# Performance work log

Measured on AMD Instinct MI355X. Metric: run time of the kernel, lower is better.

The kernel has to match this reference:

```python
import jax, jax.numpy as jnp
import numpy as np

L, B, T, I, H, P, O = 2, 64, 512, 512, 512, 256, 512


def setup_inputs() -> dict:
    key = jax.random.key(0)
    ks = iter(jax.random.split(key, 40))
    SCALE = 0.03  # keep gate pre-activations in a sane range

    def w(shape):
        return jax.random.normal(next(ks), shape, jnp.float32) * SCALE

    return {
        "x": jax.random.normal(next(ks), (B, T, I), jnp.float32),
        "Wr": w((L, H, I + H)), "br": jnp.zeros((L, H), jnp.float32),
        "Wu": w((L, H, I + H)), "bu": jnp.ones((L, H), jnp.float32),  # update_gate bias init to 1.0
        "Wn": w((L, H, I + H)), "bn": jnp.zeros((L, H), jnp.float32),
        "Wmr": w((L, P, H)), "bmr": jnp.zeros((L, P), jnp.float32),
        "Wmw": w((L, P, H)), "bmw": jnp.zeros((L, P), jnp.float32),
        "Wmu": w((L, P, H)), "bmu": jnp.zeros((L, P), jnp.float32),
        "Wmh": w((L, H, P)), "bmh": jnp.zeros((L, H), jnp.float32),
        "Wd": w((L, P, H)), "bd": jnp.zeros((L, P), jnp.float32),
        "Ws": w((L, P, H)), "bs": jnp.zeros((L, P), jnp.float32),
        "Wout": w((O, H)), "bout": jnp.zeros((O,), jnp.float32),
        "dopamine": jnp.full((1,), 0.5, jnp.float32),
        "serotonin": jnp.full((1,), 0.5, jnp.float32),
    }


def _lin(x, W, b):
    # x: [B, in], W: [out, in] (torch Linear layout), b: [out]
    return jnp.einsum("bi,oi->bo", x, W) + b


def reference(x, Wr, br, Wu, bu, Wn, bn, Wmr, bmr, Wmw, bmw, Wmu, bmu,
              Wmh, bmh, Wd, bd, Ws, bs, Wout, bout, dopamine, serotonin):
    num_layers = Wr.shape[0]
    bsz = x.shape[0]
    hdim = Wr.shape[1]
    pdim = Wmr.shape[1]
    h0 = jnp.zeros((num_layers, bsz, hdim), x.dtype)
    m0 = jnp.zeros((num_layers, bsz, pdim), x.dtype)

    def step(carry, x_t):
        hidden, memory = carry  # [L,B,H], [L,B,P]
        inp = x_t
        new_h, new_m = [], []
        for l in range(num_layers):
            h, m = hidden[l], memory[l]
            comb = jnp.concatenate([inp, h], axis=-1)
            reset = jax.nn.sigmoid(_lin(comb, Wr[l], br[l]))
            update = jax.nn.sigmoid(_lin(comb, Wu[l], bu[l]))
            comb_r = jnp.concatenate([inp, reset * h], axis=-1)
            new_hid = jnp.tanh(_lin(comb_r, Wn[l], bn[l]))
            h_cand = (1.0 - update) * h + update * new_hid
            read_gate = jax.nn.sigmoid(_lin(h_cand, Wmr[l], bmr[l]))
            mem_out = read_gate * m
            h_mem = h_cand + _lin(mem_out, Wmh[l], bmh[l])
            write_gate = jax.nn.sigmoid(_lin(h_mem, Wmw[l], bmw[l]))
            new_mem_content = jnp.tanh(_lin(h_mem, Wmu[l], bmu[l]))
            dopa = jax.nn.sigmoid(_lin(h_mem, Wd[l], bd[l]) * dopamine)
            write_gate = write_gate * dopa
            sero = jax.nn.sigmoid(_lin(h_mem, Ws[l], bs[l]) * serotonin)
            write_gate = write_gate * (1.0 - sero)
            m_new = (1.0 - write_gate) * m + write_gate * new_mem_content
            inp = h_mem
            new_h.append(h_mem)
            new_m.append(m_new)
        out_t = _lin(inp, Wout, bout)  # [B, O]
        return (jnp.stack(new_h), jnp.stack(new_m)), out_t

    (h_final, m_final), outs = jax.lax.scan(step, (h0, m0), jnp.swapaxes(x, 0, 1))
    outputs = jnp.swapaxes(outs, 0, 1)  # [B, T, O]
    return outputs, h_final, m_final
```

## Files before the change

### kernel.cpp

```cpp
#include <hip/hip_runtime.h>
#include <math.h>

#define BB 64
#define TT 512
#define II 512
#define HH 512
#define PP 256
#define OO 512

#define NTHR 512
#define AGT __HIP_MEMORY_SCOPE_AGENT

__device__ __align__(256) double g_h0d[2*BB*HH];
__device__ __align__(256) double g_h1 [BB*HH];
__device__ __align__(256) double g_rh [2*BB*HH];
__device__ __align__(256) double g_hc [2*BB*HH];
__device__ __align__(256) double g_mo [2*BB*PP];
__device__ __align__(256) double g_hist[(long)BB*TT*HH];
__device__ unsigned g_sync[2048];

__device__ __align__(256) float g_WRU [2*1024*1024];
__device__ __align__(256) float g_WnT [2*1024*512];
__device__ __align__(256) float g_WMG [2*512*1024];
__device__ __align__(256) float g_WmrT[2*512*256];
__device__ __align__(256) float g_WmhT[2*256*512];
__device__ __align__(256) float g_WoutT[512*512];

struct KP {
  const float *x,*Wr,*br,*Wu,*bu,*Wn,*bn,*Wmr,*bmr,*Wmw,*bmw,*Wmu,*bmu,
              *Wmh,*bmh,*Wd,*bd,*Ws,*bs,*Wout,*bout,*dop,*ser;
  float* out;
};

__device__ inline double sigd(double x){ return 1.0/(1.0+exp(-x)); }

__global__ void __launch_bounds__(256) prep(KP p)
{
  __shared__ float tile[32][33];
  const int b = blockIdx.x;
  const int T_RUN = 3072;
  const int T_MG  = T_RUN + 1024;
  const int T_MR  = T_MG  + 256;
  const int T_MH  = T_MR  + 256;
  const int T_OUT = T_MH  + 256;
  const int tid = threadIdx.x;

  const float* src = nullptr; float* dst = nullptr;
  int K=0, C=0, st=1, off=0, k0=0, c0=0;
  bool xpose = true;

  if (b < T_RUN){
    int m = b >> 10, r = b & 1023, l = r >> 9, t = r & 511;
    K=1024; C=512; int ct = t & 15, kt = t >> 4; k0=kt*32; c0=ct*32;
    src = (m==0? p.Wr : m==1? p.Wu : p.Wn) + (long)l*C*K;
    if (m<2){ dst = g_WRU + (long)l*1024*1024; st=2; off=m; }
    else    { dst = g_WnT + (long)l*1024*512;  st=1; off=0; }
  } else if (b < T_MG){
    int q = b - T_RUN, m = q >> 8, r = q & 255, l = r >> 7, t = r & 127;
    K=512; C=256; int ct = t & 7, kt = t >> 3; k0=kt*32; c0=ct*32;
    const float* s4[4] = {p.Wmw,p.Wmu,p.Wd,p.Ws};
    src = s4[m] + (long)l*C*K;
    dst = g_WMG + (long)l*512*1024; st=4; off=m;
  } else if (b < T_MR){
    int r = b - T_MG, l = r >> 7, t = r & 127;
    K=512; C=256; int ct = t & 7, kt = t >> 3; k0=kt*32; c0=ct*32;
    src = p.Wmr + (long)l*C*K;
    dst = g_WmrT + (long)l*512*256; st=1; off=0;
  } else if (b < T_MH){
    int r = b - T_MR, l = r >> 7, t = r & 127;
    K=256; C=512; int ct = t & 15, kt = t >> 4; k0=kt*32; c0=ct*32;
    src = p.Wmh + (long)l*C*K;
    dst = g_WmhT + (long)l*256*512; st=1; off=0;
  } else if (b < T_OUT){
    int t = b - T_MH;
    K=512; C=512; int ct = t & 15, kt = t >> 4; k0=kt*32; c0=ct*32;
    src = p.Wout; dst = g_WoutT; st=1; off=0;
  } else {
    xpose = false;
    long i = (long)(b - T_OUT)*256 + tid;
    if (i < 2L*BB*HH) g_h0d[i] = 0.0;
    if (i < (long)BB*HH) g_h1[i] = 0.0;
    if (i < 2048) g_sync[(int)i] = 0u;
  }

  if (xpose){
    for (int i=tid; i<1024; i+=256){
      int ty=i>>5, tx=i&31;
      tile[ty][tx] = src[(long)(c0+ty)*K + k0+tx];
    }
    __syncthreads();
    for (int i=tid; i<1024; i+=256){
      int ky=i>>5, cx=i&31;
      dst[(long)(k0+ky)*C*st + (long)(c0+cx)*st + off] = tile[cx][ky];
    }
  }
}

__global__ void __launch_bounds__(NTHR) rnn_kernel(KP p)
{
  const int tid  = threadIdx.x;
  const int xcd  = blockIdx.x & 7;
  const int lay  = xcd >> 2;
  const int xl   = xcd & 3;
  const int cs   = (blockIdx.x >> 3) & 3;
  const int rb   = blockIdx.x >> 5;
  const int row  = tid >> 6;
  const int lane = tid & 63;
  const int r0g  = rb*8;
  const int colH0 = xl*128 + cs*32;
  const int colP0 = xl*64  + cs*16;

  __shared__ double sP[8][512];
  __shared__ double sH[8][512];
  __shared__ double sB[8][512];
  __shared__ double sM[8][256];
  __shared__ double su[8][32];
  __shared__ double sm[8][16];

  if (tid < 128) sm[tid>>4][tid&15] = 0.0;

  const float* WRU = g_WRU  + (long)lay*1024*1024;
  const float* WN  = g_WnT  + (long)lay*1024*512;
  const float* WMGp= g_WMG  + (long)lay*512*1024;
  const float* WMR = g_WmrT + (long)lay*512*256;
  const float* WMH = g_WmhT + (long)lay*256*512;
  const float* br_ = p.br + lay*HH; const float* bu_ = p.bu + lay*HH;
  const float* bn_ = p.bn + lay*HH; const float* bmh_= p.bmh+ lay*HH;
  const float* bmr_= p.bmr+ lay*PP; const float* bmw_= p.bmw+ lay*PP;
  const float* bmu_= p.bmu+ lay*PP; const float* bd_ = p.bd + lay*PP;
  const float* bs_ = p.bs + lay*PP;
  const double dopa = (double)p.dop[0];
  const double sero = (double)p.ser[0];

  double* rhG = g_rh + (long)lay*BB*HH + (long)r0g*HH;
  double* hcG = g_hc + (long)lay*BB*HH + (long)r0g*HH;
  double* moG = g_mo + (long)lay*BB*PP + (long)r0g*PP;

  auto bidx = [&](int l, int s){ return (((rb<<1)|l)<<2 | s)<<5; };

  auto bar = [&](int s){
    __syncthreads();
    if (tid==0){
      unsigned* cnt = &g_sync[bidx(lay,s)];
      unsigned* gen = cnt + 16;
      unsigned ge  = __hip_atomic_load(gen,__ATOMIC_RELAXED,AGT);
      unsigned old = __hip_atomic_fetch_add(cnt,1u,__ATOMIC_RELEASE,AGT);
      if (old==15u){
        __hip_atomic_store(cnt,0u,__ATOMIC_RELAXED,AGT);
        __hip_atomic_fetch_add(gen,1u,__ATOMIC_RELEASE,AGT);
      } else {
        while(__hip_atomic_load(gen,__ATOMIC_RELAXED,AGT)==ge) __builtin_amdgcn_s_sleep(1);
      }
      asm volatile("" ::: "memory");
    }
    __syncthreads();
  };
  auto wait_ge = [&](int l, int s, unsigned v){
    if (tid==0){
      unsigned* gen = &g_sync[bidx(l,s)] + 16;
      while(__hip_atomic_load(gen,__ATOMIC_RELAXED,AGT) < v) __builtin_amdgcn_s_sleep(1);
      asm volatile("" ::: "memory");
    }
    __syncthreads();
  };

  auto ld512 = [&](double dst[8][512], const double* src){
    double v[8];
    #pragma unroll
    for (int j=0;j<8;++j) v[j] = __hip_atomic_load(src + (long)j*HH + tid, __ATOMIC_RELAXED, AGT);
    #pragma unroll
    for (int j=0;j<8;++j) dst[j][tid] = v[j];
  };
  auto ld256 = [&](const double* src){
    double v[4];
    #pragma unroll
    for (int j=0;j<4;++j){
      int idx = j*512 + tid;
      v[j] = __hip_atomic_load(src + (long)(idx>>8)*PP + (idx&255), __ATOMIC_RELAXED, AGT);
    }
    #pragma unroll
    for (int j=0;j<4;++j){
      int idx = j*512 + tid;
      sM[idx>>8][idx&255] = v[j];
    }
  };
  auto ldX = [&](int t){
    float v[8];
    #pragma unroll
    for (int j=0;j<8;++j) v[j] = p.x[((long)(r0g+j)*TT + t)*II + tid];
    #pragma unroll
    for (int j=0;j<8;++j) sP[j][tid] = (double)v[j];
  };

  auto ruS = [&](){
    const int c = lane&31, ks = lane>>5;
    const int col = colH0 + c;
    const float* w = WRU + (long)(ks*512)*1024 + col*2;
    const double* a = ks ? &sH[row][0] : &sP[row][0];
    double r0=0,r1=0,u0=0,u1=0;
    #pragma unroll 8
    for (int k=0;k<512;k+=2){
      double2 av = *(const double2*)(a+k);
      float2 w0 = *(const float2*)(w + (long)k*1024);
      float2 w1 = *(const float2*)(w + (long)(k+1)*1024);
      r0 = fma(av.x,(double)w0.x,r0); u0 = fma(av.x,(double)w0.y,u0);
      r1 = fma(av.y,(double)w1.x,r1); u1 = fma(av.y,(double)w1.y,u1);
    }
    double orr=r0+r1, ouu=u0+u1;
    orr += __shfl_xor(orr,32); ouu += __shfl_xor(ouu,32);
    if (lane<32){
      double r = sigd(orr + (double)br_[col]);
      double u = sigd(ouu + (double)bu_[col]);
      su[row][c] = u;
      __hip_atomic_store(&rhG[(long)row*HH+col], r*sH[row][col], __ATOMIC_RELAXED, AGT);
    }
  };
  auto mgS = [&](){
    const int pc = lane&15, ks = lane>>4;
    const int pcol = colP0 + pc;
    const float* w4 = WMGp + (long)(ks*128)*1024 + pcol*4;
    const double* a = &sH[row][ks*128];
    double q0=0,q1=0,q2=0,q3=0;
    #pragma unroll 8
    for (int k=0;k<128;++k){
      int kk = (k + (ks<<2)) & 127;
      double av = a[kk];
      float4 v = *(const float4*)(w4 + (long)kk*1024);
      q0=fma(av,(double)v.x,q0); q1=fma(av,(double)v.y,q1);
      q2=fma(av,(double)v.z,q2); q3=fma(av,(double)v.w,q3);
    }
    q0+=__shfl_xor(q0,16); q0+=__shfl_xor(q0,32);
    q1+=__shfl_xor(q1,16); q1+=__shfl_xor(q1,32);
    q2+=__shfl_xor(q2,16); q2+=__shfl_xor(q2,32);
    q3+=__shfl_xor(q3,16); q3+=__shfl_xor(q3,32);
    if (lane<16){
      double wg = sigd(q0 + (double)bmw_[pcol]);
      double nm = tanh(q1 + (double)bmu_[pcol]);
      double dp = sigd((q2 + (double)bd_[pcol])*dopa);
      double sr = sigd((q3 + (double)bs_[pcol])*sero);
      double ww = wg*dp*(1.0 - sr);
      sm[row][pc] = (1.0-ww)*sm[row][pc] + ww*nm;
    }
  };
  auto nS = [&](){
    const int c = lane&31, ks = lane>>5;
    const int col = colH0 + c;
    const float* w = WN + (long)(ks*512)*512 + col;
    const double* a = ks ? &sB[row][0] : &sP[row][0];
    double a0=0,a1=0,a2=0,a3=0;
    #pragma unroll 4
    for (int k=0;k<512;k+=4){
      double2 v0 = *(const double2*)(a+k), v1 = *(const double2*)(a+k+2);
      a0 = fma(v0.x,(double)w[(long)k*512],    a0);
      a1 = fma(v0.y,(double)w[(long)(k+1)*512],a1);
      a2 = fma(v1.x,(double)w[(long)(k+2)*512],a2);
      a3 = fma(v1.y,(double)w[(long)(k+3)*512],a3);
    }
    double o = (a0+a1)+(a2+a3);
    o += __shfl_xor(o,32);
    if (lane<32){
      double nh = tanh(o + (double)bn_[col]);
      double u = su[row][c];
      __hip_atomic_store(&hcG[(long)row*HH+col],
        (1.0-u)*sH[row][col] + u*nh, __ATOMIC_RELAXED, AGT);
    }
  };
  auto rgS = [&](){
    const int pc = lane&15, ks = lane>>4;
    const int pcol = colP0 + pc;
    const float* w = WMR + (long)(ks*128)*256 + pcol;
    const double* a = &sB[row][ks*128];
    double o=0,o2=0;
    #pragma unroll 8
    for (int k=0;k<128;k+=2){
      int ka = (k   + (ks<<2)) & 127;
      int kb = (k+1 + (ks<<2)) & 127;
      o  = fma(a[ka],(double)w[(long)ka*256],o);
      o2 = fma(a[kb],(double)w[(long)kb*256],o2);
    }
    o += o2; o += __shfl_xor(o,16); o += __shfl_xor(o,32);
    if (lane<16){
      __hip_atomic_store(&moG[(long)row*PP+pcol],
        sigd(o + (double)bmr_[pcol]) * sm[row][pc], __ATOMIC_RELAXED, AGT);
    }
  };
  auto hmS = [&](int t){
    const int c = lane&31, ks = lane>>5;
    const int col = colH0 + c;
    const float* w = WMH + (long)(ks*128)*512 + col;
    const double* a = &sM[row][ks*128];
    double o=0,o2=0;
    #pragma unroll 8
    for (int k=0;k<128;k+=2){
      o  = fma(a[k],  (double)w[(long)k*512],    o);
      o2 = fma(a[k+1],(double)w[(long)(k+1)*512],o2);
    }
    o += o2; o += __shfl_xor(o,32);
    if (lane<32){
      double hv = o + (double)bmh_[col] + sB[row][col];
      long gi = (long)(r0g+row)*HH + col;
      if (lay==0){
        __hip_atomic_store(&g_h0d[(long)(t&1)*BB*HH + gi], hv, __ATOMIC_RELAXED, AGT);
      } else {
        __hip_atomic_store(&g_h1[gi], hv, __ATOMIC_RELAXED, AGT);
        __builtin_nontemporal_store(hv, &g_hist[((long)(r0g+row)*TT + t)*HH + col]);
      }
    }
  };

  for (int t=0; t<TT; ++t){
    if (lay==0){
      ldX(t);
      ld512(sH, &g_h0d[(long)((t+1)&1)*BB*HH + (long)r0g*HH]);
    } else {
      wait_ge(0,3,(unsigned)(t+1));
      ld512(sP, &g_h0d[(long)(t&1)*BB*HH + (long)r0g*HH]);
      ld512(sH, g_h1 + (long)r0g*HH);
    }
    __syncthreads();
    ruS();
    if (t>0) mgS();
    bar(0);
    ld512(sB, rhG);
    __syncthreads();
    nS();
    bar(1);
    ld512(sB, hcG);
    __syncthreads();
    rgS();
    bar(2);
    ld256(moG);
    __syncthreads();
    if (lay==0 && t>=2) wait_ge(1,0,(unsigned)(t-1));
    hmS(t);
    bar(3);
  }

  if (lay==0) ld512(sH, &g_h0d[(long)((TT-1)&1)*BB*HH + (long)r0g*HH]);
  else        ld512(sH, g_h1 + (long)r0g*HH);
  __syncthreads();
  mgS();
  __syncthreads();

  const long ob = (long)BB*TT*OO;
  if (tid < 256){
    int r = tid>>5, c = tid&31; int col = colH0 + c; long bq = r0g + r;
    p.out[ob + (long)lay*BB*HH + bq*HH + col] = (float)sH[r][col];
  }
  if (tid < 128){
    int r = tid>>4, pc = tid&15; int pcol = colP0 + pc; long bq = r0g + r;
    p.out[ob + 2L*BB*HH + (long)lay*BB*PP + bq*PP + pcol] = (float)sm[r][pc];
  }
}

__global__ void __launch_bounds__(512) out_gemm(const float* bout, float* out)
{
  __shared__ double sH[8][512];
  const int tid = threadIdx.x;
  const int iw = tid >> 6, lane = tid & 63;
  const int kq = lane >> 5, c32 = lane & 31;
  const int col = iw*64 + c32*2;
  const float* w = g_WoutT + kq*(256*512) + col;
  for (int rbx = blockIdx.x; rbx < BB*TT/8; rbx += gridDim.x){
    __syncthreads();
    for (int i = tid; i < 8*256; i += 512){
      int rr = i >> 8, c2 = (i & 255) << 1;
      *(double2*)&sH[rr][c2] = *(const double2*)(g_hist + (long)(rbx*8+rr)*HH + c2);
    }
    __syncthreads();
    double s[8][2];
    #pragma unroll
    for (int r=0;r<8;++r){ s[r][0]=0.0; s[r][1]=0.0; }
    #pragma unroll 2
    for (int k=0;k<256;++k){
      float2 wv = *(const float2*)(w + (long)k*512);
      double wx = (double)wv.x, wy = (double)wv.y;
      #pragma unroll
      for (int r=0;r<8;++r){
        double av = sH[r][kq*256 + k];
        s[r][0] = fma(av, wx, s[r][0]);
        s[r][1] = fma(av, wy, s[r][1]);
      }
    }
    #pragma unroll
    for (int r=0;r<8;++r){
      double t0 = s[r][0] + __shfl_xor(s[r][0],32);
      double t1 = s[r][1] + __shfl_xor(s[r][1],32);
      if (lane < 32){
        float2 fv;
        fv.x = (float)(t0 + (double)bout[col]);
        fv.y = (float)(t1 + (double)bout[col+1]);
        *(float2*)&out[(long)(rbx*8+r)*OO + col] = fv;
      }
    }
  }
}

extern "C" void kernel_launch(void* const* d_in, const int* in_sizes, int n_in,
                              void* d_out, int out_size, void* d_ws, size_t ws_size,
                              hipStream_t stream)
{
  KP p;
  p.x   = (const float*)d_in[0];
  p.Wr  = (const float*)d_in[1];  p.br  = (const float*)d_in[2];
  p.Wu  = (const float*)d_in[3];  p.bu  = (const float*)d_in[4];
  p.Wn  = (const float*)d_in[5];  p.bn  = (const float*)d_in[6];
  p.Wmr = (const float*)d_in[7];  p.bmr = (const float*)d_in[8];
  p.Wmw = (const float*)d_in[9];  p.bmw = (const float*)d_in[10];
  p.Wmu = (const float*)d_in[11]; p.bmu = (const float*)d_in[12];
  p.Wmh = (const float*)d_in[13]; p.bmh = (const float*)d_in[14];
  p.Wd  = (const float*)d_in[15]; p.bd  = (const float*)d_in[16];
  p.Ws  = (const float*)d_in[17]; p.bs  = (const float*)d_in[18];
  p.Wout= (const float*)d_in[19]; p.bout= (const float*)d_in[20];
  p.dop = (const float*)d_in[21]; p.ser = (const float*)d_in[22];
  p.out = (float*)d_out;

  prep<<<dim3(5120), dim3(256), 0, stream>>>(p);
  rnn_kernel<<<dim3(256), dim3(NTHR), 0, stream>>>(p);
  out_gemm<<<dim3(2048), dim3(512), 0, stream>>>(p.bout, p.out);
}
```

Baseline: 57.57 ms.

## Spread recurrent kernel over 512 blocks with 4 rows each and double-precision weights

Halves batch rows per block (8 to 4) and doubles the grid to 512 blocks, so each wave computes half a row's columns with a deeper k-split and extra shuffle reductions. Several weight copies (WRU, Wmr, Wmh, Wout) are pre-converted to double in prep to drop per-FMA conversions. Shared arrays are padded to reduce bank conflicts. The aim is more parallelism per sequential step, at the cost of doubled weight bandwidth for the double copies and more blocks taking part in each grid barrier.

Result: slower. 115.0 ms (+99.7%).

```diff
diff --git a/kernel.cpp b/kernel.cpp
--- a/kernel.cpp
+++ b/kernel.cpp
@@ -8,7 +8,9 @@
 #define PP 256
 #define OO 512
 
+#define NBLK 512
 #define NTHR 512
+#define RPB 4
 #define AGT __HIP_MEMORY_SCOPE_AGENT
 
 __device__ __align__(256) double g_h0d[2*BB*HH];
@@ -17,14 +19,14 @@
 __device__ __align__(256) double g_hc [2*BB*HH];
 __device__ __align__(256) double g_mo [2*BB*PP];
 __device__ __align__(256) double g_hist[(long)BB*TT*HH];
-__device__ unsigned g_sync[2048];
-
-__device__ __align__(256) float g_WRU [2*1024*1024];
-__device__ __align__(256) float g_WnT [2*1024*512];
-__device__ __align__(256) float g_WMG [2*512*1024];
-__device__ __align__(256) float g_WmrT[2*512*256];
-__device__ __align__(256) float g_WmhT[2*256*512];
-__device__ __align__(256) float g_WoutT[512*512];
+__device__ unsigned g_sync[4096];
+
+__device__ __align__(256) double g_WRUd [2L*1024*1024];
+__device__ __align__(256) float  g_WnT  [2*1024*512];
+__device__ __align__(256) float  g_WMG  [2*512*1024];
+__device__ __align__(256) double g_WmrTd[2*512*256];
+__device__ __align__(256) double g_WmhTd[2*256*512];
+__device__ __align__(256) double g_WoutTd[512*512];
 
 struct KP {
   const float *x,*Wr,*br,*Wu,*bu,*Wn,*bn,*Wmr,*bmr,*Wmw,*bmw,*Wmu,*bmu,
@@ -45,85 +47,85 @@
   const int T_OUT = T_MH  + 256;
   const int tid = threadIdx.x;
 
-  const float* src = nullptr; float* dst = nullptr;
-  int K=0, C=0, st=1, off=0, k0=0, c0=0;
-  bool xpose = true;
+  const float* src=nullptr; void* dstv=nullptr;
+  int K=0,C=0,st=1,off=0,k0=0,c0=0,dt=0;
+  bool xpose=true;
 
   if (b < T_RUN){
-    int m = b >> 10, r = b & 1023, l = r >> 9, t = r & 511;
-    K=1024; C=512; int ct = t & 15, kt = t >> 4; k0=kt*32; c0=ct*32;
+    int m=b>>10, r=b&1023, l=r>>9, t=r&511;
+    K=1024; C=512; int ct=t&15, kt=t>>4; k0=kt*32; c0=ct*32;
     src = (m==0? p.Wr : m==1? p.Wu : p.Wn) + (long)l*C*K;
-    if (m<2){ dst = g_WRU + (long)l*1024*1024; st=2; off=m; }
-    else    { dst = g_WnT + (long)l*1024*512;  st=1; off=0; }
+    if (m<2){ dstv = g_WRUd + (long)l*1024*1024; st=2; off=m; dt=1; }
+    else    { dstv = g_WnT  + (long)l*1024*512;  st=1; off=0; dt=0; }
   } else if (b < T_MG){
-    int q = b - T_RUN, m = q >> 8, r = q & 255, l = r >> 7, t = r & 127;
-    K=512; C=256; int ct = t & 7, kt = t >> 3; k0=kt*32; c0=ct*32;
-    const float* s4[4] = {p.Wmw,p.Wmu,p.Wd,p.Ws};
+    int q=b-T_RUN, m=q>>8, r=q&255, l=r>>7, t=r&127;
+    K=512; C=256; int ct=t&7, kt=t>>3; k0=kt*32; c0=ct*32;
+    const float* s4[4]={p.Wmw,p.Wmu,p.Wd,p.Ws};
     src = s4[m] + (long)l*C*K;
-    dst = g_WMG + (long)l*512*1024; st=4; off=m;
+    dstv = g_WMG + (long)l*512*1024; st=4; off=m; dt=0;
   } else if (b < T_MR){
-    int r = b - T_MG, l = r >> 7, t = r & 127;
-    K=512; C=256; int ct = t & 7, kt = t >> 3; k0=kt*32; c0=ct*32;
+    int r=b-T_MG, l=r>>7, t=r&127;
+    K=512; C=256; int ct=t&7, kt=t>>3; k0=kt*32; c0=ct*32;
     src = p.Wmr + (long)l*C*K;
-    dst = g_WmrT + (long)l*512*256; st=1; off=0;
+    dstv = g_WmrTd + (long)l*512*256; st=1; off=0; dt=1;
   } else if (b < T_MH){
-    int r = b - T_MR, l = r >> 7, t = r & 127;
-    K=256; C=512; int ct = t & 15, kt = t >> 4; k0=kt*32; c0=ct*32;
+    int r=b-T_MR, l=r>>7, t=r&127;
+    K=256; C=512; int ct=t&15, kt=t>>4; k0=kt*32; c0=ct*32;
     src = p.Wmh + (long)l*C*K;
-    dst = g_WmhT + (long)l*256*512; st=1; off=0;
+    dstv = g_WmhTd + (long)l*256*512; st=1; off=0; dt=1;
   } else if (b < T_OUT){
-    int t = b - T_MH;
-    K=512; C=512; int ct = t & 15, kt = t >> 4; k0=kt*32; c0=ct*32;
-    src = p.Wout; dst = g_WoutT; st=1; off=0;
+    int t=b-T_MH;
+    K=512; C=512; int ct=t&15, kt=t>>4; k0=kt*32; c0=ct*32;
+    src = p.Wout; dstv = g_WoutTd; st=1; off=0; dt=1;
   } else {
-    xpose = false;
-    long i = (long)(b - T_OUT)*256 + tid;
-    if (i < 2L*BB*HH) g_h0d[i] = 0.0;
-    if (i < (long)BB*HH) g_h1[i] = 0.0;
-    if (i < 2048) g_sync[(int)i] = 0u;
+    xpose=false;
+    long i = (long)(b-T_OUT)*256 + tid;
+    if (i < 2L*BB*HH) g_h0d[i]=0.0;
+    if (i < (long)BB*HH) g_h1[i]=0.0;
+    if (i < 4096) g_sync[(int)i]=0u;
   }
 
   if (xpose){
-    for (int i=tid; i<1024; i+=256){
+    for (int i=tid;i<1024;i+=256){
       int ty=i>>5, tx=i&31;
       tile[ty][tx] = src[(long)(c0+ty)*K + k0+tx];
     }
     __syncthreads();
-    for (int i=tid; i<1024; i+=256){
+    for (int i=tid;i<1024;i+=256){
       int ky=i>>5, cx=i&31;
-      dst[(long)(k0+ky)*C*st + (long)(c0+cx)*st + off] = tile[cx][ky];
+      long o = (long)(k0+ky)*C*st + (long)(c0+cx)*st + off;
+      if (dt) ((double*)dstv)[o] = (double)tile[cx][ky];
+      else    ((float*)dstv)[o]  = tile[cx][ky];
     }
   }
 }
 
-__global__ void __launch_bounds__(NTHR) rnn_kernel(KP p)
+__global__ void __launch_bounds__(NTHR,4) rnn_kernel(KP p)
 {
-  const int tid  = threadIdx.x;
-  const int xcd  = blockIdx.x & 7;
-  const int lay  = xcd >> 2;
-  const int xl   = xcd & 3;
-  const int cs   = (blockIdx.x >> 3) & 3;
-  const int rb   = blockIdx.x >> 5;
-  const int row  = tid >> 6;
-  const int lane = tid & 63;
-  const int r0g  = rb*8;
-  const int colH0 = xl*128 + cs*32;
-  const int colP0 = xl*64  + cs*16;
-
-  __shared__ double sP[8][512];
-  __shared__ double sH[8][512];
-  __shared__ double sB[8][512];
-  __shared__ double sM[8][256];
-  __shared__ double su[8][32];
-  __shared__ double sm[8][16];
-
-  if (tid < 128) sm[tid>>4][tid&15] = 0.0;
-
-  const float* WRU = g_WRU  + (long)lay*1024*1024;
-  const float* WN  = g_WnT  + (long)lay*1024*512;
-  const float* WMGp= g_WMG  + (long)lay*512*1024;
-  const float* WMR = g_WmrT + (long)lay*512*256;
-  const float* WMH = g_WmhT + (long)lay*256*512;
+  const int tid=threadIdx.x;
+  const int xcd=blockIdx.x&7, lay=xcd>>2, xl=xcd&3;
+  const int cs=(blockIdx.x>>3)&3, rb=blockIdx.x>>5;
+  const int iw=tid>>6, row=iw>>1, ch=iw&1, lane=tid&63;
+  const int r0g=rb*RPB;
+  const int colH0=xl*128+cs*32, colP0=xl*64+cs*16;
+  const int cbase=colH0+ch*16, pbase=colP0+ch*8;
+
+  __shared__ double sP[RPB][520];
+  __shared__ double sH[RPB][520];
+  __shared__ double sB[RPB][520];
+  __shared__ double sM[RPB][264];
+  __shared__ double su[RPB][32];
+  __shared__ double sm[RPB][16];
+
+  if (tid<64) sm[tid>>4][tid&15]=0.0;
+
+  auto fs=[](int k){ return k + ((k>>7)<<1); };
+
+  const double* WRU = g_WRUd + (long)lay*1024*1024;
+  const float*  WN  = g_WnT  + (long)lay*1024*512;
+  const float*  WMGp= g_WMG  + (long)lay*512*1024;
+  const double* WMR = g_WmrTd+ (long)lay*512*256;
+  const double* WMH = g_WmhTd+ (long)lay*256*512;
   const float* br_ = p.br + lay*HH; const float* bu_ = p.bu + lay*HH;
   const float* bn_ = p.bn + lay*HH; const float* bmh_= p.bmh+ lay*HH;
   const float* bmr_= p.bmr+ lay*PP; const float* bmw_= p.bmw+ lay*PP;
@@ -136,15 +138,14 @@
   double* hcG = g_hc + (long)lay*BB*HH + (long)r0g*HH;
   double* moG = g_mo + (long)lay*BB*PP + (long)r0g*PP;
 
-  auto bidx = [&](int l, int s){ return (((rb<<1)|l)<<2 | s)<<5; };
-
-  auto bar = [&](int s){
+  const int gidx = rb*2 + lay;
+  auto bar=[&](int s){
     __syncthreads();
     if (tid==0){
-      unsigned* cnt = &g_sync[bidx(lay,s)];
-      unsigned* gen = cnt + 16;
-      unsigned ge  = __hip_atomic_load(gen,__ATOMIC_RELAXED,AGT);
-      unsigned old = __hip_atomic_fetch_add(cnt,1u,__ATOMIC_RELEASE,AGT);
+      unsigned* cnt=&g_sync[(gidx*4+s)*32];
+      unsigned* gen=cnt+16;
+      unsigned ge=__hip_atomic_load(gen,__ATOMIC_RELAXED,AGT);
+      unsigned old=__hip_atomic_fetch_add(cnt,1u,__ATOMIC_RELEASE,AGT);
       if (old==15u){
         __hip_atomic_store(cnt,0u,__ATOMIC_RELAXED,AGT);
         __hip_atomic_fetch_add(gen,1u,__ATOMIC_RELEASE,AGT);
@@ -155,155 +156,169 @@
     }
     __syncthreads();
   };
-  auto wait_ge = [&](int l, int s, unsigned v){
+  auto wait_ge=[&](int l,int s,unsigned v){
     if (tid==0){
-      unsigned* gen = &g_sync[bidx(l,s)] + 16;
-      while(__hip_atomic_load(gen,__ATOMIC_RELAXED,AGT) < v) __builtin_amdgcn_s_sleep(1);
+      unsigned* gen=&g_sync[((rb*2+l)*4+s)*32+16];
+      while(__hip_atomic_load(gen,__ATOMIC_RELAXED,AGT)<v) __builtin_amdgcn_s_sleep(1);
       asm volatile("" ::: "memory");
     }
     __syncthreads();
   };
 
-  auto ld512 = [&](double dst[8][512], const double* src){
-    double v[8];
-    #pragma unroll
-    for (int j=0;j<8;++j) v[j] = __hip_atomic_load(src + (long)j*HH + tid, __ATOMIC_RELAXED, AGT);
-    #pragma unroll
-    for (int j=0;j<8;++j) dst[j][tid] = v[j];
-  };
-  auto ld256 = [&](const double* src){
+  auto ld512=[&](double dst[RPB][520], const double* src){
     double v[4];
     #pragma unroll
     for (int j=0;j<4;++j){
-      int idx = j*512 + tid;
-      v[j] = __hip_atomic_load(src + (long)(idx>>8)*PP + (idx&255), __ATOMIC_RELAXED, AGT);
+      int idx=j*512+tid;
+      v[j]=__hip_atomic_load(src + (long)(idx>>9)*HH + (idx&511), __ATOMIC_RELAXED, AGT);
     }
     #pragma unroll
     for (int j=0;j<4;++j){
-      int idx = j*512 + tid;
-      sM[idx>>8][idx&255] = v[j];
-    }
-  };
-  auto ldX = [&](int t){
-    float v[8];
-    #pragma unroll
-    for (int j=0;j<8;++j) v[j] = p.x[((long)(r0g+j)*TT + t)*II + tid];
-    #pragma unroll
-    for (int j=0;j<8;++j) sP[j][tid] = (double)v[j];
-  };
-
-  auto ruS = [&](){
-    const int c = lane&31, ks = lane>>5;
-    const int col = colH0 + c;
-    const float* w = WRU + (long)(ks*512)*1024 + col*2;
-    const double* a = ks ? &sH[row][0] : &sP[row][0];
-    double r0=0,r1=0,u0=0,u1=0;
-    #pragma unroll 8
-    for (int k=0;k<512;k+=2){
-      double2 av = *(const double2*)(a+k);
-      float2 w0 = *(const float2*)(w + (long)k*1024);
-      float2 w1 = *(const float2*)(w + (long)(k+1)*1024);
-      r0 = fma(av.x,(double)w0.x,r0); u0 = fma(av.x,(double)w0.y,u0);
-      r1 = fma(av.y,(double)w1.x,r1); u1 = fma(av.y,(double)w1.y,u1);
-    }
-    double orr=r0+r1, ouu=u0+u1;
-    orr += __shfl_xor(orr,32); ouu += __shfl_xor(ouu,32);
-    if (lane<32){
-      double r = sigd(orr + (double)br_[col]);
-      double u = sigd(ouu + (double)bu_[col]);
-      su[row][c] = u;
-      __hip_atomic_store(&rhG[(long)row*HH+col], r*sH[row][col], __ATOMIC_RELAXED, AGT);
-    }
-  };
-  auto mgS = [&](){
-    const int pc = lane&15, ks = lane>>4;
-    const int pcol = colP0 + pc;
-    const float* w4 = WMGp + (long)(ks*128)*1024 + pcol*4;
-    const double* a = &sH[row][ks*128];
+      int idx=j*512+tid; int c=idx&511;
+      dst[idx>>9][c + ((c>>7)<<1)] = v[j];
+    }
+  };
+  auto ld256=[&](const double* src){
+    double v[2];
+    #pragma unroll
+    for (int j=0;j<2;++j){
+      int idx=j*512+tid;
+      v[j]=__hip_atomic_load(src + (long)(idx>>8)*PP + (idx&255), __ATOMIC_RELAXED, AGT);
+    }
+    #pragma unroll
+    for (int j=0;j<2;++j){
+      int idx=j*512+tid; int c=idx&255;
+      sM[idx>>8][c + ((c>>6)<<1)] = v[j];
+    }
+  };
+  auto ldX=[&](int t){
+    float v[4];
+    #pragma unroll
+    for (int j=0;j<4;++j){
+      int idx=j*512+tid;
+      v[j]=p.x[((long)(r0g+(idx>>9))*TT + t)*II + (idx&511)];
+    }
+    #pragma unroll
+    for (int j=0;j<4;++j){
+      int idx=j*512+tid; int c=idx&511;
+      sP[idx>>9][c + ((c>>7)<<1)] = (double)v[j];
+    }
+  };
+
+  auto ruS=[&](){
+    const int c=lane&15, ks=lane>>4;
+    const int col=cbase+c;
+    const double* w = WRU + (long)(ks*256)*1024 + col*2;
+    const double* a = (ks<2)? &sP[row][260*ks] : &sH[row][260*(ks-2)];
+    double racc=0,uacc=0;
+    #pragma unroll 2
+    for (int h=0;h<2;++h){
+      const double* ah = a + h*130;
+      const double* wh = w + (long)h*128*1024;
+      #pragma unroll 8
+      for (int k=0;k<128;++k){
+        double av=ah[k];
+        double2 wv=*(const double2*)(wh + (long)k*1024);
+        racc=fma(av,wv.x,racc); uacc=fma(av,wv.y,uacc);
+      }
+    }
+    racc+=__shfl_xor(racc,16); racc+=__shfl_xor(racc,32);
+    uacc+=__shfl_xor(uacc,16); uacc+=__shfl_xor(uacc,32);
+    if (lane<16){
+      double r=sigd(racc+(double)br_[col]);
+      double u=sigd(uacc+(double)bu_[col]);
+      su[row][ch*16+c]=u;
+      __hip_atomic_store(&rhG[(long)row*HH+col], r*sH[row][fs(col)], __ATOMIC_RELAXED, AGT);
+    }
+  };
+  auto nS=[&](){
+    const int c=lane&15, ks=lane>>4;
+    const int col=cbase+c;
+    const float* w = WN + (long)(ks*256)*512 + col;
+    const double* a = (ks<2)? &sP[row][260*ks] : &sB[row][260*(ks-2)];
+    double acc=0,acc2=0;
+    #pragma unroll 2
+    for (int h=0;h<2;++h){
+      const double* ah=a+h*130;
+      const float* wh=w+(long)h*128*512;
+      #pragma unroll 8
+      for (int k=0;k<128;k+=2){
+        acc =fma(ah[k],  (double)wh[(long)k*512],    acc);
+        acc2=fma(ah[k+1],(double)wh[(long)(k+1)*512],acc2);
+      }
+    }
+    double o=acc+acc2;
+    o+=__shfl_xor(o,16); o+=__shfl_xor(o,32);
+    if (lane<16){
+      double nh=tanh(o+(double)bn_[col]);
+      double u=su[row][ch*16+c];
+      __hip_atomic_store(&hcG[(long)row*HH+col],
+        (1.0-u)*sH[row][fs(col)]+u*nh, __ATOMIC_RELAXED, AGT);
+    }
+  };
+  auto mgS=[&](){
+    const int pc=lane&7, ks=lane>>3;
+    const int pcol=pbase+pc;
+    const float* w4 = WMGp + (long)(ks*64)*1024 + pcol*4;
+    const double* a = &sH[row][ks*64 + ((ks>>1)<<1)];
     double q0=0,q1=0,q2=0,q3=0;
     #pragma unroll 8
-    for (int k=0;k<128;++k){
-      int kk = (k + (ks<<2)) & 127;
-      double av = a[kk];
-      float4 v = *(const float4*)(w4 + (long)kk*1024);
+    for (int k=0;k<64;++k){
+      double av=a[k];
+      float4 v=*(const float4*)(w4 + (long)k*1024);
       q0=fma(av,(double)v.x,q0); q1=fma(av,(double)v.y,q1);
       q2=fma(av,(double)v.z,q2); q3=fma(av,(double)v.w,q3);
     }
-    q0+=__shfl_xor(q0,16); q0+=__shfl_xor(q0,32);
-    q1+=__shfl_xor(q1,16); q1+=__shfl_xor(q1,32);
-    q2+=__shfl_xor(q2,16); q2+=__shfl_xor(q2,32);
-    q3+=__shfl_xor(q3,16); q3+=__shfl_xor(q3,32);
-    if (lane<16){
-      double wg = sigd(q0 + (double)bmw_[pcol]);
-      double nm = tanh(q1 + (double)bmu_[pcol]);
-      double dp = sigd((q2 + (double)bd_[pcol])*dopa);
-      double sr = sigd((q3 + (double)bs_[pcol])*sero);
-      double ww = wg*dp*(1.0 - sr);
-      sm[row][pc] = (1.0-ww)*sm[row][pc] + ww*nm;
-    }
-  };
-  auto nS = [&](){
-    const int c = lane&31, ks = lane>>5;
-    const int col = colH0 + c;
-    const float* w = WN + (long)(ks*512)*512 + col;
-    const double* a = ks ? &sB[row][0] : &sP[row][0];
-    double a0=0,a1=0,a2=0,a3=0;
-    #pragma unroll 4
-    for (int k=0;k<512;k+=4){
-      double2 v0 = *(const double2*)(a+k), v1 = *(const double2*)(a+k+2);
-      a0 = fma(v0.x,(double)w[(long)k*512],    a0);
-      a1 = fma(v0.y,(double)w[(long)(k+1)*512],a1);
-      a2 = fma(v1.x,(double)w[(long)(k+2)*512],a2);
-      a3 = fma(v1.y,(double)w[(long)(k+3)*512],a3);
-    }
-    double o = (a0+a1)+(a2+a3);
-    o += __shfl_xor(o,32);
-    if (lane<32){
-      double nh = tanh(o + (double)bn_[col]);
-      double u = su[row][c];
-      __hip_atomic_store(&hcG[(long)row*HH+col],
-        (1.0-u)*sH[row][col] + u*nh, __ATOMIC_RELAXED, AGT);
-    }
-  };
-  auto rgS = [&](){
-    const int pc = lane&15, ks = lane>>4;
-    const int pcol = colP0 + pc;
-    const float* w = WMR + (long)(ks*128)*256 + pcol;
-    const double* a = &sB[row][ks*128];
+    q0+=__shfl_xor(q0,8); q0+=__shfl_xor(q0,16); q0+=__shfl_xor(q0,32);
+    q1+=__shfl_xor(q1,8); q1+=__shfl_xor(q1,16); q1+=__shfl_xor(q1,32);
+    q2+=__shfl_xor(q2,8); q2+=__shfl_xor(q2,16); q2+=__shfl_xor(q2,32);
+    q3+=__shfl_xor(q3,8); q3+=__shfl_xor(q3,16); q3+=__shfl_xor(q3,32);
+    if (lane<8){
+      double wg=sigd(q0+(double)bmw_[pcol]);
+      double nm=tanh(q1+(double)bmu_[pcol]);
+      double dp=sigd((q2+(double)bd_[pcol])*dopa);
+      double sr=sigd((q3+(double)bs_[pcol])*sero);
+      double ww=wg*dp*(1.0-sr);
+      sm[row][ch*8+pc]=(1.0-ww)*sm[row][ch*8+pc]+ww*nm;
+    }
+  };
+  auto rgS=[&](){
+    const int pc=lane&7, ks=lane>>3;
+    const int pcol=pbase+pc;
+    const double* w = WMR + (long)(ks*64)*256 + pcol;
+    const double* a = &sB[row][ks*64 + ((ks>>1)<<1)];
     double o=0,o2=0;
     #pragma unroll 8
-    for (int k=0;k<128;k+=2){
-      int ka = (k   + (ks<<2)) & 127;
-      int kb = (k+1 + (ks<<2)) & 127;
-      o  = fma(a[ka],(double)w[(long)ka*256],o);
-      o2 = fma(a[kb],(double)w[(long)kb*256],o2);
-    }
-    o += o2; o += __shfl_xor(o,16); o += __shfl_xor(o,32);
-    if (lane<16){
+    for (int k=0;k<64;k+=2){
+      o =fma(a[k],  w[(long)k*256],    o);
+      o2=fma(a[k+1],w[(long)(k+1)*256],o2);
+    }
+    o+=o2; o+=__shfl_xor(o,8); o+=__shfl_xor(o,16); o+=__shfl_xor(o,32);
+    if (lane<8){
       __hip_atomic_store(&moG[(long)row*PP+pcol],
-        sigd(o + (double)bmr_[pcol]) * sm[row][pc], __ATOMIC_RELAXED, AGT);
-    }
-  };
-  auto hmS = [&](int t){
-    const int c = lane&31, ks = lane>>5;
-    const int col = colH0 + c;
-    const float* w = WMH + (long)(ks*128)*512 + col;
-    const double* a = &sM[row][ks*128];
+        sigd(o+(double)bmr_[pcol])*sm[row][ch*8+pc], __ATOMIC_RELAXED, AGT);
+    }
+  };
+  auto hmS=[&](int t){
+    const int c=lane&15, ks=lane>>4;
+    const int col=cbase+c;
+    const double* w = WMH + (long)(ks*64)*512 + col;
+    const double* a = &sM[row][66*ks];
     double o=0,o2=0;
     #pragma unroll 8
-    for (int k=0;k<128;k+=2){
-      o  = fma(a[k],  (double)w[(long)k*512],    o);
-      o2 = fma(a[k+1],(double)w[(long)(k+1)*512],o2);
-    }
-    o += o2; o += __shfl_xor(o,32);
-    if (lane<32){
-      double hv = o + (double)bmh_[col] + sB[row][col];
-      long gi = (long)(r0g+row)*HH + col;
+    for (int k=0;k<64;k+=2){
+      o =fma(a[k],  w[(long)k*512],    o);
+      o2=fma(a[k+1],w[(long)(k+1)*512],o2);
+    }
+    o+=o2; o+=__shfl_xor(o,16); o+=__shfl_xor(o,32);
+    if (lane<16){
+      double hv = o + (double)bmh_[col] + sB[row][fs(col)];
+      long gi=(long)(r0g+row)*HH+col;
       if (lay==0){
-        __hip_atomic_store(&g_h0d[(long)(t&1)*BB*HH + gi], hv, __ATOMIC_RELAXED, AGT);
+        __hip_atomic_store(&g_h0d[(long)(t&1)*BB*HH+gi],hv,__ATOMIC_RELAXED,AGT);
       } else {
-        __hip_atomic_store(&g_h1[gi], hv, __ATOMIC_RELAXED, AGT);
-        __builtin_nontemporal_store(hv, &g_hist[((long)(r0g+row)*TT + t)*HH + col]);
+        __hip_atomic_store(&g_h1[gi],hv,__ATOMIC_RELAXED,AGT);
+        __builtin_nontemporal_store(hv,&g_hist[((long)(r0g+row)*TT+t)*HH+col]);
       }
     }
   };
@@ -342,13 +357,13 @@
   mgS();
   __syncthreads();
 
-  const long ob = (long)BB*TT*OO;
-  if (tid < 256){
-    int r = tid>>5, c = tid&31; int col = colH0 + c; long bq = r0g + r;
-    p.out[ob + (long)lay*BB*HH + bq*HH + col] = (float)sH[r][col];
-  }
-  if (tid < 128){
-    int r = tid>>4, pc = tid&15; int pcol = colP0 + pc; long bq = r0g + r;
+  const long ob=(long)BB*TT*OO;
+  if (tid<128){
+    int r=tid>>5, c=tid&31; int col=colH0+c; long bq=r0g+r;
+    p.out[ob + (long)lay*BB*HH + bq*HH + col] = (float)sH[r][fs(col)];
+  }
+  if (tid<64){
+    int r=tid>>4, pc=tid&15; int pcol=colP0+pc; long bq=r0g+r;
     p.out[ob + 2L*BB*HH + (long)lay*BB*PP + bq*PP + pcol] = (float)sm[r][pc];
   }
 }
@@ -360,7 +375,7 @@
   const int iw = tid >> 6, lane = tid & 63;
   const int kq = lane >> 5, c32 = lane & 31;
   const int col = iw*64 + c32*2;
-  const float* w = g_WoutT + kq*(256*512) + col;
+  const double* w = g_WoutTd + kq*(256*512) + col;
   for (int rbx = blockIdx.x; rbx < BB*TT/8; rbx += gridDim.x){
     __syncthreads();
     for (int i = tid; i < 8*256; i += 512){
@@ -373,13 +388,12 @@
     for (int r=0;r<8;++r){ s[r][0]=0.0; s[r][1]=0.0; }
     #pragma unroll 2
     for (int k=0;k<256;++k){
-      float2 wv = *(const float2*)(w + (long)k*512);
-      double wx = (double)wv.x, wy = (double)wv.y;
+      double2 wv = *(const double2*)(w + (long)k*512);
       #pragma unroll
       for (int r=0;r<8;++r){
         double av = sH[r][kq*256 + k];
-        s[r][0] = fma(av, wx, s[r][0]);
-        s[r][1] = fma(av, wy, s[r][1]);
+        s[r][0] = fma(av, wv.x, s[r][0]);
+        s[r][1] = fma(av, wv.y, s[r][1]);
       }
     }
     #pragma unroll
@@ -416,6 +430,6 @@
   p.out = (float*)d_out;
 
   prep<<<dim3(5120), dim3(256), 0, stream>>>(p);
-  rnn_kernel<<<dim3(256), dim3(NTHR), 0, stream>>>(p);
+  rnn_kernel<<<dim3(NBLK), dim3(NTHR), 0, stream>>>(p);
   out_gemm<<<dim3(2048), dim3(512), 0, stream>>>(p.bout, p.out);
 }
```
